# Optimization experiments

Hardware: AMD Instinct MI355X
Metric: run time of the kernel (lower is better)

Reference implementation:

```python
import jax, jax.numpy as jnp
import numpy as np

LOWER_T = 6.0
UPPER_T = 50.0


def _conv(x, w, pad_h, pad_w):
    # x: [N,1,H,W] or [N,Cin,H,W]; w: [O,I,kh,kw]; cross-correlation like torch Conv2d
    return jax.lax.conv_general_dilated(
        x, w, window_strides=(1, 1),
        padding=[(pad_h, pad_h), (pad_w, pad_w)],
        dimension_numbers=('NCHW', 'OIHW', 'NCHW'))


def setup_inputs() -> dict:
    key = jax.random.key(0)
    H = W = 4096
    img = jax.random.uniform(key, (1, 3, H, W), dtype=jnp.float32) * 255.0

    # scipy.signal.gaussian(5, std=1.0), unnormalized window
    std = 1.0
    g = np.exp(-0.5 * ((np.arange(5, dtype=np.float32) - 2.0) / std) ** 2).astype(np.float32)
    gauss = jnp.asarray(g)  # [5]

    sobel = jnp.asarray(np.array([[1, 0, -1], [2, 0, -2], [1, 0, -1]], dtype=np.float32))  # [3,3]

    f = np.zeros((8, 1, 3, 3), dtype=np.float32)
    f[:, 0, 1, 1] = 1.0
    offs = [(1, 2), (2, 2), (2, 1), (2, 0), (1, 0), (0, 0), (0, 1), (0, 2)]  # 0,45,...,315 deg
    for k, (r, c) in enumerate(offs):
        f[k, 0, r, c] = -1.0
    dir_w = jnp.asarray(f)  # [8,1,3,3]

    return {"img": img, "gauss": gauss, "sobel": sobel, "dir_w": dir_w}


def reference(img, gauss, sobel, dir_w):
    N, C, H, W = img.shape  # N == 1, C == 3
    x = img.reshape(C, 1, H, W)  # treat channels as batch

    # separable gaussian blur: 1x5 then 5x1, padding 2 (matches torch Conv2d)
    gw_h = gauss.reshape(1, 1, 1, 5)
    gw_v = gauss.reshape(1, 1, 5, 1)
    blurred = _conv(_conv(x, gw_h, 0, 2), gw_v, 2, 0)  # [3,1,H,W]

    sw_h = sobel.reshape(1, 1, 3, 3)
    sw_v = sobel.T.reshape(1, 1, 3, 3)
    gx = _conv(blurred, sw_h, 1, 1)  # [3,1,H,W]
    gy = _conv(blurred, sw_v, 1, 1)

    # per-channel magnitude summed over RGB -> [1,1,H,W]
    grad_mag = jnp.sqrt(gx * gx + gy * gy + 1e-8).sum(axis=0, keepdims=True)[:, 0:1]

    gx_sum = gx.sum(axis=0, keepdims=True)[:, 0:1]
    gy_sum = gy.sum(axis=0, keepdims=True)[:, 0:1]
    ori = jnp.arctan2(gy_sum, gx_sum) * (180.0 / 3.14159) + 180.0
    ori = jnp.round(ori / 45.0) * 45.0

    all_filtered = _conv(grad_mag, dir_w, 1, 1)  # [1,8,H,W]

    idx_pos = jnp.mod(ori / 45.0, 8.0).astype(jnp.int32)          # [1,1,H,W]
    idx_neg = jnp.mod(ori / 45.0 + 4.0, 8.0).astype(jnp.int32)

    cs_pos = jnp.take_along_axis(all_filtered, idx_pos, axis=1)  # [1,1,H,W]
    cs_neg = jnp.take_along_axis(all_filtered, idx_neg, axis=1)

    is_max = jnp.minimum(cs_pos, cs_neg) > 0.0

    thin = jnp.where(is_max, grad_mag, 0.0)
    keep = is_max & (thin >= LOWER_T) & (thin <= UPPER_T)
    thresholded = jnp.where(keep, 1.0, 0.0).astype(jnp.float32)  # [1,1,H,W]
    return thresholded
```

## Files before the change

kernel.cpp:

```cpp
#include <hip/hip_runtime.h>


#define IMG_H 4096
#define IMG_W 4096

constexpr int TW = 32, TH = 32;
constexpr int HBH = 40, HBW = 44;
constexpr int BH  = 36, BW  = 44;
constexpr int MH  = 34, MW  = 36;

__device__ __forceinline__ void stageD(
    const float* __restrict__ s_bs, const float* __restrict__ s_mg,
    float* __restrict__ out, int X0, int Y0, int tid) {
  const int ty  = tid >> 3;
  const int tx0 = (tid & 7) << 2;
  const int row1 = (ty + 1) * MW;

  float4 q0 = *(const float4*)&s_mg[row1 + tx0];
  float4 q1 = *(const float4*)&s_mg[row1 + tx0 + 4];
  float mcs[4];
  mcs[0] = q0.y; mcs[1] = q0.z; mcs[2] = q0.w; mcs[3] = q1.x;

  bool band = false;
#pragma unroll
  for (int e = 0; e < 4; ++e)
    band = band || (mcs[e] >= 6.0f && mcs[e] <= 50.0f);

  float4 resv = make_float4(0.f, 0.f, 0.f, 0.f);
  if (__ballot(band) != 0ULL) {
    float w0[8], w1[8], w2[8];
#pragma unroll
    for (int rr = 0; rr < 3; ++rr) {
      float* w = (rr == 0) ? w0 : (rr == 1) ? w1 : w2;
      float4 p = *(const float4*)&s_bs[(ty + 1 + rr) * BW + tx0];
      float4 q = *(const float4*)&s_bs[(ty + 1 + rr) * BW + tx0 + 4];
      w[0]=p.x; w[1]=p.y; w[2]=p.z; w[3]=p.w; w[4]=q.x; w[5]=q.y; w[6]=q.z; w[7]=q.w;
    }
    const unsigned long long off_tbl = 0xDDDCDBFF23242501ULL;
    float res[4];
#pragma unroll
    for (int e = 0; e < 4; ++e) {
      int tx = tx0 + e;
      float b00 = w0[e + 1], b01 = w0[e + 2], b02 = w0[e + 3];
      float b10 = w1[e + 1],                  b12 = w1[e + 3];
      float b20 = w2[e + 1], b21 = w2[e + 2], b22 = w2[e + 3];
      float gxs = b00 - b02 + 2.f * b10 - 2.f * b12 + b20 - b22;
      float gys = b00 + 2.f * b01 + b02 - b20 - 2.f * b21 - b22;
      float ax = fabsf(gxs), ay = fabsf(gys);
      float f1 = ay - 0.41421356f * ax;
      float f2 = ay - 2.4142137f * ax;
      int off;
      if (fminf(fabsf(f1), fabsf(f2)) < 1e-4f * (ax + ay)) {
        float ori = atan2f(gys, gxs) * 57.295827908797776f + 180.0f;
        int k = (int)rintf(ori / 45.0f);
        int ip = k & 7;
        off = (int)(signed char)(off_tbl >> (ip * 8));
      } else {
        off = (f1 <= 0.f) ? 1
            : (f2 >= 0.f) ? MW
            : (((__float_as_uint(gxs) ^ __float_as_uint(gys)) >> 31) ? (MW - 1)
                                                                     : (MW + 1));
      }
      int ctr = row1 + (tx + 1);
      float mc  = mcs[e];
      float csp = mc - s_mg[ctr + off];
      float csn = mc - s_mg[ctr - off];
      bool is_max = fminf(csp, csn) > 0.0f;
      bool keep = is_max && (mc >= 6.0f) && (mc <= 50.0f);
      res[e] = keep ? 1.0f : 0.0f;
    }
    resv = make_float4(res[0], res[1], res[2], res[3]);
  }
  *(float4*)&out[(size_t)(Y0 + ty) * IMG_W + (X0 + tx0)] = resv;
}

__device__ __forceinline__ void pipeline_interior(
    const float* __restrict__ img,
    float g0, float g1, float g2, float g3, float g4,
    int X0, int Y0, int tid,
    float* __restrict__ s_hb, float* __restrict__ s_bl,
    float* __restrict__ s_bs, float* __restrict__ s_mg,
    float* __restrict__ out) {

  const int rA0 = tid / 10, cA0 = (tid - rA0 * 10) * 4;
  const int jA1 = tid + 256;
  const int rA1 = jA1 / 10, cA1 = (jA1 - rA1 * 10) * 4;
  const bool hasA1 = (tid < 144);

  float4 pa0, pb0, pa1, pb1;

  auto issueA = [&](int ch) {
    const float* im = img + (size_t)ch * ((size_t)IMG_H * IMG_W);
    const float* r0 = im + (size_t)(Y0 - 4 + rA0) * IMG_W + (X0 - 4 + cA0);
    pa0 = *(const float4*)r0;
    pb0 = *(const float4*)(r0 + 4);
    if (hasA1) {
      const float* r1 = im + (size_t)(Y0 - 4 + rA1) * IMG_W + (X0 - 4 + cA1);
      pa1 = *(const float4*)r1;
      pb1 = *(const float4*)(r1 + 4);
    }
  };
  auto storeA = [&]() {
    auto h5 = [&](const float4& a, const float4& b) {
      float4 o;
      o.x = g0 * a.x + g1 * a.y + g2 * a.z + g3 * a.w + g4 * b.x;
      o.y = g0 * a.y + g1 * a.z + g2 * a.w + g3 * b.x + g4 * b.y;
      o.z = g0 * a.z + g1 * a.w + g2 * b.x + g3 * b.y + g4 * b.z;
      o.w = g0 * a.w + g1 * b.x + g2 * b.y + g3 * b.z + g4 * b.w;
      return o;
    };
    *(float4*)&s_hb[rA0 * HBW + cA0] = h5(pa0, pb0);
    if (hasA1) *(float4*)&s_hb[rA1 * HBW + cA1] = h5(pa1, pb1);
  };

  auto stageB = [&](int ch) {
    for (int j = tid; j < BH * 10; j += 256) {
      int r = j / 10, g = j - r * 10;
      int c0 = g * 4;
      const float* p = &s_hb[r * HBW + c0];
      float4 a0 = *(const float4*)(p);
      float4 a1 = *(const float4*)(p + HBW);
      float4 a2 = *(const float4*)(p + 2 * HBW);
      float4 a3 = *(const float4*)(p + 3 * HBW);
      float4 a4 = *(const float4*)(p + 4 * HBW);
      float4 v;
      v.x = g0 * a0.x + g1 * a1.x + g2 * a2.x + g3 * a3.x + g4 * a4.x;
      v.y = g0 * a0.y + g1 * a1.y + g2 * a2.y + g3 * a3.y + g4 * a4.y;
      v.z = g0 * a0.z + g1 * a1.z + g2 * a2.z + g3 * a3.z + g4 * a4.z;
      v.w = g0 * a0.w + g1 * a1.w + g2 * a2.w + g3 * a3.w + g4 * a4.w;
      *(float4*)&s_bl[r * BW + c0] = v;
      float4* ps = (float4*)&s_bs[r * BW + c0];
      if (ch == 0) {
        *ps = v;
      } else {
        float4 s = *ps;
        s.x += v.x; s.y += v.y; s.z += v.z; s.w += v.w;
        *ps = s;
      }
    }
  };

  auto stageC = [&](int ch) {
    for (int j = tid; j < MH * 9; j += 256) {
      int r = j / 9, g = j - r * 9;
      int c0 = g * 4;
      float w0[6], w1[6], w2[6];
      const float* p = &s_bl[r * BW + c0];
      { float4 a = *(const float4*)(p);          float2 b = *(const float2*)(p + 4);
        w0[0]=a.x; w0[1]=a.y; w0[2]=a.z; w0[3]=a.w; w0[4]=b.x; w0[5]=b.y; }
      { float4 a = *(const float4*)(p + BW);     float2 b = *(const float2*)(p + BW + 4);
        w1[0]=a.x; w1[1]=a.y; w1[2]=a.z; w1[3]=a.w; w1[4]=b.x; w1[5]=b.y; }
      { float4 a = *(const float4*)(p + 2 * BW); float2 b = *(const float2*)(p + 2 * BW + 4);
        w2[0]=a.x; w2[1]=a.y; w2[2]=a.z; w2[3]=a.w; w2[4]=b.x; w2[5]=b.y; }
      float res[4];
#pragma unroll
      for (int e = 0; e < 4; ++e) {
        float gxv = w0[e] - w0[e + 2] + 2.f * w1[e] - 2.f * w1[e + 2] + w2[e] - w2[e + 2];
        float gyv = w0[e] + 2.f * w0[e + 1] + w0[e + 2] - w2[e] - 2.f * w2[e + 1] - w2[e + 2];
        res[e] = sqrtf(gxv * gxv + gyv * gyv + 1e-8f);
      }
      float4* pd = (float4*)&s_mg[r * MW + c0];
      if (ch == 0) {
        *pd = make_float4(res[0], res[1], res[2], res[3]);
      } else {
        float4 s = *pd;
        s.x += res[0]; s.y += res[1]; s.z += res[2]; s.w += res[3];
        *pd = s;
      }
    }
  };

  issueA(0);
  storeA();
  __syncthreads();
#pragma unroll
  for (int ch = 0; ch < 3; ++ch) {
    stageB(ch);
    __syncthreads();
    if (ch < 2) issueA(ch + 1);
    stageC(ch);
    if (ch < 2) storeA();
    __syncthreads();
  }
  stageD(s_bs, s_mg, out, X0, Y0, tid);
}

__device__ void pipeline_boundary(
    const float* __restrict__ img,
    float g0, float g1, float g2, float g3, float g4,
    int X0, int Y0, int tid,
    float* __restrict__ s_hb, float* __restrict__ s_bl,
    float* __restrict__ s_bs, float* __restrict__ s_mg,
    float* __restrict__ out) {

  for (int ch = 0; ch < 3; ++ch) {
    const float* im = img + (size_t)ch * ((size_t)IMG_H * IMG_W);

    for (int j = tid; j < HBH * 10; j += 256) {
      int r = j / 10, g = j - r * 10;
      int c0 = g * 4;
      int gy = Y0 - 4 + r;
      float4 o;
      if ((unsigned)gy < IMG_H) {
        int cb = X0 - 4 + c0;
        const float* row = im + (size_t)gy * IMG_W;
        float a0, a1, a2, a3, a4, a5, a6, a7;
        if (cb >= 0 && cb + 7 < IMG_W) {
          float4 va = *(const float4*)(row + cb);
          float4 vb = *(const float4*)(row + cb + 4);
          a0 = va.x; a1 = va.y; a2 = va.z; a3 = va.w;
          a4 = vb.x; a5 = vb.y; a6 = vb.z; a7 = vb.w;
        } else {
          float t[8];
#pragma unroll
          for (int u = 0; u < 8; ++u) {
            int x = cb + u;
            t[u] = ((unsigned)x < IMG_W) ? row[x] : 0.f;
          }
          a0 = t[0]; a1 = t[1]; a2 = t[2]; a3 = t[3];
          a4 = t[4]; a5 = t[5]; a6 = t[6]; a7 = t[7];
        }
        o.x = g0 * a0 + g1 * a1 + g2 * a2 + g3 * a3 + g4 * a4;
        o.y = g0 * a1 + g1 * a2 + g2 * a3 + g3 * a4 + g4 * a5;
        o.z = g0 * a2 + g1 * a3 + g2 * a4 + g3 * a5 + g4 * a6;
        o.w = g0 * a3 + g1 * a4 + g2 * a5 + g3 * a6 + g4 * a7;
      } else {
        o = make_float4(0.f, 0.f, 0.f, 0.f);
      }
      *(float4*)&s_hb[r * HBW + c0] = o;
    }
    __syncthreads();

    for (int j = tid; j < BH * 10; j += 256) {
      int r = j / 10, g = j - r * 10;
      int c0 = g * 4;
      const float* p = &s_hb[r * HBW + c0];
      float4 a0 = *(const float4*)(p);
      float4 a1 = *(const float4*)(p + HBW);
      float4 a2 = *(const float4*)(p + 2 * HBW);
      float4 a3 = *(const float4*)(p + 3 * HBW);
      float4 a4 = *(const float4*)(p + 4 * HBW);
      float4 v;
      v.x = g0 * a0.x + g1 * a1.x + g2 * a2.x + g3 * a3.x + g4 * a4.x;
      v.y = g0 * a0.y + g1 * a1.y + g2 * a2.y + g3 * a3.y + g4 * a4.y;
      v.z = g0 * a0.z + g1 * a1.z + g2 * a2.z + g3 * a3.z + g4 * a4.z;
      v.w = g0 * a0.w + g1 * a1.w + g2 * a2.w + g3 * a3.w + g4 * a4.w;
      {
        int gy = Y0 - 2 + r;
        bool rok = (unsigned)gy < IMG_H;
        int gx0 = X0 - 2 + c0;
        v.x = (rok && (unsigned)(gx0    ) < IMG_W) ? v.x : 0.f;
        v.y = (rok && (unsigned)(gx0 + 1) < IMG_W) ? v.y : 0.f;
        v.z = (rok && (unsigned)(gx0 + 2) < IMG_W) ? v.z : 0.f;
        v.w = (rok && (unsigned)(gx0 + 3) < IMG_W) ? v.w : 0.f;
      }
      *(float4*)&s_bl[r * BW + c0] = v;
      float4* ps = (float4*)&s_bs[r * BW + c0];
      if (ch == 0) {
        *ps = v;
      } else {
        float4 s = *ps;
        s.x += v.x; s.y += v.y; s.z += v.z; s.w += v.w;
        *ps = s;
      }
    }
    __syncthreads();

    for (int j = tid; j < MH * 9; j += 256) {
      int r = j / 9, g = j - r * 9;
      int c0 = g * 4;
      float w0[6], w1[6], w2[6];
      const float* p = &s_bl[r * BW + c0];
      { float4 a = *(const float4*)(p);          float2 b = *(const float2*)(p + 4);
        w0[0]=a.x; w0[1]=a.y; w0[2]=a.z; w0[3]=a.w; w0[4]=b.x; w0[5]=b.y; }
      { float4 a = *(const float4*)(p + BW);     float2 b = *(const float2*)(p + BW + 4);
        w1[0]=a.x; w1[1]=a.y; w1[2]=a.z; w1[3]=a.w; w1[4]=b.x; w1[5]=b.y; }
      { float4 a = *(const float4*)(p + 2 * BW); float2 b = *(const float2*)(p + 2 * BW + 4);
        w2[0]=a.x; w2[1]=a.y; w2[2]=a.z; w2[3]=a.w; w2[4]=b.x; w2[5]=b.y; }
      float res[4];
#pragma unroll
      for (int e = 0; e < 4; ++e) {
        float gxv = w0[e] - w0[e + 2] + 2.f * w1[e] - 2.f * w1[e + 2] + w2[e] - w2[e + 2];
        float gyv = w0[e] + 2.f * w0[e + 1] + w0[e + 2] - w2[e] - 2.f * w2[e + 1] - w2[e + 2];
        float m = sqrtf(gxv * gxv + gyv * gyv + 1e-8f);
        int gy = Y0 - 1 + r;
        int gx = X0 - 1 + c0 + e;
        res[e] = ((unsigned)gy < IMG_H && (unsigned)gx < IMG_W) ? m : 0.f;
      }
      float4* pd = (float4*)&s_mg[r * MW + c0];
      if (ch == 0) {
        *pd = make_float4(res[0], res[1], res[2], res[3]);
      } else {
        float4 s = *pd;
        s.x += res[0]; s.y += res[1]; s.z += res[2]; s.w += res[3];
        *pd = s;
      }
    }
    __syncthreads();
  }
  stageD(s_bs, s_mg, out, X0, Y0, tid);
}

__global__ __launch_bounds__(256, 6)
void canny_fused(const float* __restrict__ img,
                 const float* __restrict__ gauss,
                 float* __restrict__ out) {
  __shared__ float s_hb[HBH * HBW];
  __shared__ float s_bl[BH * BW];
  __shared__ float s_bs[BH * BW];
  __shared__ float s_mg[MH * MW];

  const int tid = threadIdx.x;
  const int X0 = blockIdx.x * TW;
  const int Y0 = blockIdx.y * TH;
  const float g0 = gauss[0], g1 = gauss[1], g2 = gauss[2],
              g3 = gauss[3], g4 = gauss[4];

  const bool interior = (blockIdx.x >= 1) && (blockIdx.x <= 126) &&
                        (blockIdx.y >= 1) && (blockIdx.y <= 126);
  if (interior)
    pipeline_interior(img, g0, g1, g2, g3, g4, X0, Y0, tid, s_hb, s_bl, s_bs, s_mg, out);
  else
    pipeline_boundary(img, g0, g1, g2, g3, g4, X0, Y0, tid, s_hb, s_bl, s_bs, s_mg, out);
}

extern "C" void kernel_launch(void* const* d_in, const int* in_sizes, int n_in,
                              void* d_out, int out_size, void* d_ws, size_t ws_size,
                              hipStream_t stream) {
  const float* img   = (const float*)d_in[0];
  const float* gauss = (const float*)d_in[1];
  float* out = (float*)d_out;
  dim3 grid(IMG_W / TW, IMG_H / TH);
  canny_fused<<<grid, 256, 0, stream>>>(img, gauss, out);
}
```

Measured before the change: 336.9 us.

## Shrink shared buffers, skip sqrt for strong-gradient waves, raise occupancy

Narrows the row strides of the horizontal-blur and blurred buffers and stores the channel-summed blur only for the region stage D reads. This cuts LDS use per block so the launch bound can go from 6 to 7 blocks per CU. Stage C also skips the sqrt for a whole wavefront when every pixel's gradient lower bound max(|gx|,|gy|) exceeds the upper threshold, storing that bound in place of the magnitude. That shortcut assumes such pixels can never fall inside the threshold band. Because the summed magnitude only gets larger, this plausibly holds, but it changes the intermediate values stored in s_mg.

```diff
diff --git a/kernel.cpp b/kernel.cpp
--- a/kernel.cpp
+++ b/kernel.cpp
@@ -5,8 +5,9 @@
 #define IMG_W 4096
 
 constexpr int TW = 32, TH = 32;
-constexpr int HBH = 40, HBW = 44;
-constexpr int BH  = 36, BW  = 44;
+constexpr int HBH = 40, HBW = 40;
+constexpr int BH  = 36, BW  = 40;
+constexpr int SBH = 34, SBW = 36;
 constexpr int MH  = 34, MW  = 36;
 
 __device__ __forceinline__ void stageD(
@@ -32,8 +33,8 @@
 #pragma unroll
     for (int rr = 0; rr < 3; ++rr) {
       float* w = (rr == 0) ? w0 : (rr == 1) ? w1 : w2;
-      float4 p = *(const float4*)&s_bs[(ty + 1 + rr) * BW + tx0];
-      float4 q = *(const float4*)&s_bs[(ty + 1 + rr) * BW + tx0 + 4];
+      float4 p = *(const float4*)&s_bs[(ty + rr) * SBW + tx0];
+      float4 q = *(const float4*)&s_bs[(ty + rr) * SBW + tx0 + 4];
       w[0]=p.x; w[1]=p.y; w[2]=p.z; w[3]=p.w; w[4]=q.x; w[5]=q.y; w[6]=q.z; w[7]=q.w;
     }
     const unsigned long long off_tbl = 0xDDDCDBFF23242501ULL;
@@ -129,13 +130,15 @@
       v.z = g0 * a0.z + g1 * a1.z + g2 * a2.z + g3 * a3.z + g4 * a4.z;
       v.w = g0 * a0.w + g1 * a1.w + g2 * a2.w + g3 * a3.w + g4 * a4.w;
       *(float4*)&s_bl[r * BW + c0] = v;
-      float4* ps = (float4*)&s_bs[r * BW + c0];
-      if (ch == 0) {
-        *ps = v;
-      } else {
-        float4 s = *ps;
-        s.x += v.x; s.y += v.y; s.z += v.z; s.w += v.w;
-        *ps = s;
+      if ((unsigned)(r - 1) < (unsigned)SBH && c0 < SBW) {
+        float4* ps = (float4*)&s_bs[(r - 1) * SBW + c0];
+        if (ch == 0) {
+          *ps = v;
+        } else {
+          float4 s = *ps;
+          s.x += v.x; s.y += v.y; s.z += v.z; s.w += v.w;
+          *ps = s;
+        }
       }
     }
   };
@@ -152,12 +155,23 @@
         w1[0]=a.x; w1[1]=a.y; w1[2]=a.z; w1[3]=a.w; w1[4]=b.x; w1[5]=b.y; }
       { float4 a = *(const float4*)(p + 2 * BW); float2 b = *(const float2*)(p + 2 * BW + 4);
         w2[0]=a.x; w2[1]=a.y; w2[2]=a.z; w2[3]=a.w; w2[4]=b.x; w2[5]=b.y; }
+      float gxv[4], gyv[4], lb[4];
+#pragma unroll
+      for (int e = 0; e < 4; ++e) {
+        gxv[e] = w0[e] - w0[e + 2] + 2.f * w1[e] - 2.f * w1[e + 2] + w2[e] - w2[e + 2];
+        gyv[e] = w0[e] + 2.f * w0[e + 1] + w0[e + 2] - w2[e] - 2.f * w2[e + 1] - w2[e + 2];
+        lb[e] = fmaxf(fabsf(gxv[e]), fabsf(gyv[e]));
+      }
+      float lbmin = fminf(fminf(lb[0], lb[1]), fminf(lb[2], lb[3]));
       float res[4];
-#pragma unroll
-      for (int e = 0; e < 4; ++e) {
-        float gxv = w0[e] - w0[e + 2] + 2.f * w1[e] - 2.f * w1[e + 2] + w2[e] - w2[e + 2];
-        float gyv = w0[e] + 2.f * w0[e + 1] + w0[e + 2] - w2[e] - 2.f * w2[e + 1] - w2[e + 2];
-        res[e] = sqrtf(gxv * gxv + gyv * gyv + 1e-8f);
+      if (__ballot(lbmin <= 50.0f) != 0ULL) {
+#pragma unroll
+        for (int e = 0; e < 4; ++e)
+          res[e] = sqrtf(gxv[e] * gxv[e] + gyv[e] * gyv[e] + 1e-8f);
+      } else {
+#pragma unroll
+        for (int e = 0; e < 4; ++e)
+          res[e] = lb[e];
       }
       float4* pd = (float4*)&s_mg[r * MW + c0];
       if (ch == 0) {
@@ -255,13 +269,15 @@
         v.w = (rok && (unsigned)(gx0 + 3) < IMG_W) ? v.w : 0.f;
       }
       *(float4*)&s_bl[r * BW + c0] = v;
-      float4* ps = (float4*)&s_bs[r * BW + c0];
-      if (ch == 0) {
-        *ps = v;
-      } else {
-        float4 s = *ps;
-        s.x += v.x; s.y += v.y; s.z += v.z; s.w += v.w;
-        *ps = s;
+      if ((unsigned)(r - 1) < (unsigned)SBH && c0 < SBW) {
+        float4* ps = (float4*)&s_bs[(r - 1) * SBW + c0];
+        if (ch == 0) {
+          *ps = v;
+        } else {
+          float4 s = *ps;
+          s.x += v.x; s.y += v.y; s.z += v.z; s.w += v.w;
+          *ps = s;
+        }
       }
     }
     __syncthreads();
@@ -301,13 +317,13 @@
   stageD(s_bs, s_mg, out, X0, Y0, tid);
 }
 
-__global__ __launch_bounds__(256, 6)
+__global__ __launch_bounds__(256, 7)
 void canny_fused(const float* __restrict__ img,
                  const float* __restrict__ gauss,
                  float* __restrict__ out) {
   __shared__ float s_hb[HBH * HBW];
   __shared__ float s_bl[BH * BW];
-  __shared__ float s_bs[BH * BW];
+  __shared__ float s_bs[SBH * SBW];
   __shared__ float s_mg[MH * MW];
 
   const int tid = threadIdx.x;
```

Result: no change. 332.9 us (-1.2%).
